# Performance work log

Measured on AMD Instinct MI355X. Metric: run time of the kernel, lower is better.

The kernel has to match this reference:

```python
import jax, jax.numpy as jnp
import numpy as np

B, NO, NR, DIM, RNN = 64, 128, 512, 1024, 1000


def setup_inputs() -> dict:
    key = jax.random.key(0)
    ks = jax.random.split(key, 32)
    def rn(k, shape, s=0.02):
        return jax.random.normal(k, shape, dtype=jnp.float32) * s
    inp = {}
    inp['obj_labels'] = jax.random.randint(ks[0], (B, NO, 1), 0, 26)
    inp['obj_masks'] = jnp.ones((B, NO), jnp.float32)
    inp['rela_masks'] = jnp.ones((B, NR), jnp.float32)
    inp['rela_edges'] = jax.random.randint(ks[1], (B, NR, 2), 0, NO)
    inp['rela_feats'] = jax.random.normal(ks[2], (B, NR, 8), dtype=jnp.float32)
    inp['box_feats'] = jax.random.normal(ks[3], (B, NO, 5), dtype=jnp.float32)
    # parameters
    inp['emb_table'] = jax.random.uniform(ks[4], (26, 128), jnp.float32, -0.1, 0.1)
    inp['w_objfeat'] = rn(ks[5], (5, 128));        inp['b_objfeat'] = jnp.zeros((128,), jnp.float32)
    inp['w_cat'] = rn(ks[6], (256, 128));          inp['b_cat'] = jnp.zeros((128,), jnp.float32)
    inp['w_obj'] = rn(ks[7], (128, RNN));          inp['b_obj'] = jnp.zeros((RNN,), jnp.float32)
    inp['w_rela'] = rn(ks[8], (8, RNN));           inp['b_rela'] = jnp.zeros((RNN,), jnp.float32)
    inp['w_gnn'] = rn(ks[9], (3 * RNN, RNN));      inp['b_gnn'] = jnp.zeros((RNN,), jnp.float32)
    inp['w_att_obj'] = rn(ks[10], (RNN, 1));       inp['b_att_obj'] = jnp.zeros((1,), jnp.float32)
    inp['w_att_rela'] = rn(ks[11], (RNN, 1));      inp['b_att_rela'] = jnp.zeros((1,), jnp.float32)
    inp['w_read'] = rn(ks[12], (2 * RNN, DIM));    inp['b_read'] = jnp.zeros((DIM,), jnp.float32)
    inp['w_fc'] = rn(ks[13], (DIM, 32 * 14 * 6));  inp['b_fc'] = jnp.zeros((32 * 14 * 6,), jnp.float32)
    inp['wt1'] = rn(ks[14], (32, 25, 3, 3));       inp['bt1'] = jnp.zeros((25,), jnp.float32)
    inp['wt2'] = rn(ks[15], (25, 25, 3, 3));       inp['bt2'] = jnp.zeros((25,), jnp.float32)
    inp['wt3'] = rn(ks[16], (25, 25, 3, 3));       inp['bt3'] = jnp.zeros((25,), jnp.float32)
    inp['wt4'] = rn(ks[17], (25, 25, 3, 3));       inp['bt4'] = jnp.zeros((25,), jnp.float32)
    return inp


def _attn(feats, mask, w, b):
    # feats: (B, N, RNN); mask: (B, N)
    dot = (jnp.tanh(feats) @ w + b)[..., 0]              # (B, N)
    wgt = jax.nn.softmax(dot, axis=1) * mask
    wgt = wgt / jnp.sum(wgt, axis=1, keepdims=True)
    return jnp.einsum('bn,bnd->bd', wgt, feats)          # (B, RNN)


def _up2(x):
    return jnp.repeat(jnp.repeat(x, 2, axis=2), 2, axis=3)


def _convT(x, w, b):
    # torch ConvTranspose2d (stride=1, pad=0) == full-padded corr with flipped kernel
    k = jnp.transpose(w, (1, 0, 2, 3))[:, :, ::-1, ::-1]  # (out, in, 3, 3)
    y = jax.lax.conv_general_dilated(x, k, (1, 1), [(2, 2), (2, 2)],
                                     dimension_numbers=('NCHW', 'OIHW', 'NCHW'))
    return y + b[None, :, None, None]


def reference(obj_labels, obj_masks, rela_masks, rela_edges, rela_feats, box_feats,
              emb_table, w_objfeat, b_objfeat, w_cat, b_cat, w_obj, b_obj,
              w_rela, b_rela, w_gnn, b_gnn, w_att_obj, b_att_obj,
              w_att_rela, b_att_rela, w_read, b_read, w_fc, b_fc,
              wt1, bt1, wt2, bt2, wt3, bt3, wt4, bt4):
    relu = jax.nn.relu
    # embeddings (dropout = identity at inference)
    obj_embed = relu(emb_table[obj_labels])[:, :, 0, :]                   # (B, NO, 128)
    obj_f = relu(box_feats @ w_objfeat + b_objfeat)                       # (B, NO, 128)
    obj_embed = relu(jnp.concatenate([obj_f, obj_embed], -1) @ w_cat + b_cat)
    obj_vecs = relu(obj_embed @ w_obj + b_obj)                            # (B, NO, 1000)
    rela_vecs = relu(rela_feats @ w_rela + b_rela)                        # (B, NR, 1000)
    # GNN: gather endpoints, concat, linear+relu, mask
    s = jnp.take_along_axis(obj_vecs, rela_edges[:, :, 0:1], axis=1)      # (B, NR, 1000)
    o = jnp.take_along_axis(obj_vecs, rela_edges[:, :, 1:2], axis=1)
    t = jnp.concatenate([s, rela_vecs, o], axis=-1)                       # (B, NR, 3000)
    new_rela = relu(t @ w_gnn + b_gnn) * rela_masks[..., None]
    # attention pooling
    a_obj = _attn(obj_vecs, obj_masks, w_att_obj, b_att_obj)
    a_rel = _attn(new_rela, rela_masks, w_att_rela, b_att_rela)
    enc = relu(jnp.concatenate([a_obj, a_rel], axis=1) @ w_read + b_read)  # (B, DIM)
    # decoder
    x = (enc @ w_fc + b_fc).reshape(-1, 32, 14, 6)
    x = relu(_convT(_up2(x), wt1, bt1))
    x = relu(_convT(_up2(x), wt2, bt2))
    x = relu(_convT(_up2(x), wt3, bt3))
    x = relu(_convT(_up2(x), wt4, bt4))
    x = jax.nn.sigmoid(x)                                                  # (B, 25, 254, 126)
    return enc, x
```

## Files before the change

### kernel.cpp

```cpp
#include <hip/hip_runtime.h>
#include <hip/hip_bf16.h>
#include <hip/hip_fp16.h>

#define B_    64
#define NO_   128
#define NR_   512
#define RNN_  1000
#define DIM_  1024

typedef short short8 __attribute__((ext_vector_type(8)));
typedef float f32x4  __attribute__((ext_vector_type(4)));
typedef float f32x2v __attribute__((ext_vector_type(2)));
typedef float f32x4v __attribute__((ext_vector_type(4)));

static __device__ __forceinline__ float bf2f(unsigned short u) {
    union { unsigned int i; float f; } x; x.i = ((unsigned int)u) << 16; return x.f;
}
static __device__ __forceinline__ short f2bf_s(float f) {
    __hip_bfloat16 h = __float2bfloat16(f);
    return *reinterpret_cast<short*>(&h);
}

#define GLOAD_LDS16(gp, lp) \
    __builtin_amdgcn_global_load_lds((const __attribute__((address_space(1))) void*)(gp), \
                                     (__attribute__((address_space(3))) void*)(lp), 16, 0, 0)

__global__ void k_obj_embed(const int* __restrict__ labels,
                            const float* __restrict__ box_feats,
                            const float* __restrict__ emb_table,
                            const float* __restrict__ w_objfeat, const float* __restrict__ b_objfeat,
                            const float* __restrict__ w_cat, const float* __restrict__ b_cat,
                            __hip_bfloat16* __restrict__ out)
{
    const int row = blockIdx.x;
    const int tid = threadIdx.x;
    __shared__ __align__(16) float cat[256];
    __shared__ float bf[5];
    if (tid < 5) bf[tid] = box_feats[row * 5 + tid];
    __syncthreads();
    float acc = b_objfeat[tid];
#pragma unroll
    for (int k = 0; k < 5; ++k) acc += bf[k] * w_objfeat[k * 128 + tid];
    cat[tid] = fmaxf(acc, 0.f);
    const int label = labels[row];
    cat[128 + tid] = fmaxf(emb_table[label * 128 + tid], 0.f);
    __syncthreads();
    float acc2 = b_cat[tid];
#pragma unroll 4
    for (int k4 = 0; k4 < 64; ++k4) {
        const f32x4 c4 = *(const f32x4*)&cat[k4 * 4];
        acc2 += c4[0] * w_cat[(k4 * 4 + 0) * 128 + tid];
        acc2 += c4[1] * w_cat[(k4 * 4 + 1) * 128 + tid];
        acc2 += c4[2] * w_cat[(k4 * 4 + 2) * 128 + tid];
        acc2 += c4[3] * w_cat[(k4 * 4 + 3) * 128 + tid];
    }
    out[(size_t)row * 128 + tid] = __float2bfloat16(fmaxf(acc2, 0.f));
}

__global__ void k_transpose(const float* __restrict__ W, __hip_bfloat16* __restrict__ Wt,
                            int K, int N, int ldn, int Kpad)
{
    __shared__ float t[32][33];
    const int k0 = blockIdx.x * 32, n0 = blockIdx.y * 32;
    const int c = threadIdx.x & 31, r8 = threadIdx.x >> 5;
#pragma unroll
    for (int rr = r8; rr < 32; rr += 8) {
        int k = k0 + rr, n = n0 + c;
        t[rr][c] = (k < K && n < N) ? W[(size_t)k * ldn + n] : 0.f;
    }
    __syncthreads();
#pragma unroll
    for (int rr = r8; rr < 32; rr += 8)
        Wt[(size_t)(n0 + rr) * Kpad + k0 + c] = __float2bfloat16(t[c][rr]);
}

__global__ void k_weff(const float* __restrict__ w, float* __restrict__ wg, int IC, int OC)
{
    const int idx = blockIdx.x * 256 + threadIdx.x;
    if (idx >= IC * OC) return;
    const float* wp = w + (size_t)idx * 9;
    float wl[9];
#pragma unroll
    for (int k = 0; k < 9; ++k) wl[k] = wp[k];
    const float rm_[2][2][3] = {{{0.f,1.f,1.f},{1.f,0.f,0.f}},
                                {{0.f,0.f,1.f},{1.f,1.f,0.f}}};
    float* o = wg + (size_t)idx * 16;
#pragma unroll
    for (int py = 0; py < 2; ++py)
#pragma unroll
    for (int px = 0; px < 2; ++px)
#pragma unroll
    for (int r = 0; r < 2; ++r)
#pragma unroll
    for (int c = 0; c < 2; ++c) {
        float s = 0.f;
#pragma unroll
        for (int ky = 0; ky < 3; ++ky)
#pragma unroll
        for (int kx = 0; kx < 3; ++kx)
            s += rm_[py][r][ky] * rm_[px][c][kx] * wl[ky * 3 + kx];
        o[(r * 2 + c) * 4 + (py * 2 + px)] = s;
    }
}

__global__ void k_zero_border(float* __restrict__ buf, int PH, int PW, int IR0, int IR1, int IC0, int IC1)
{
    float* plane = buf + (size_t)blockIdx.x * PH * PW;
    const int tid = threadIdx.x;
    const int topN = IR0 * PW;
    for (int i = tid; i < topN; i += 256) plane[i] = 0.f;
    const int botBase = IR1 * PW, botN = (PH - IR1) * PW;
    for (int i = tid; i < botN; i += 256) plane[botBase + i] = 0.f;
    const int rows = IR1 - IR0;
    const int wL = IC0, wR = PW - IC1, wLR = wL + wR;
    const int n = rows * wLR;
    for (int i = tid; i < n; i += 256) {
        const int r = i / wLR, c = i - r * wLR;
        const int col = (c < wL) ? c : (IC1 + c - wL);
        plane[(IR0 + r) * PW + col] = 0.f;
    }
}

__global__ void k_rv(const float* __restrict__ rela_feats, const float* __restrict__ w_rela,
                     const float* __restrict__ b_rela, __hip_bfloat16* __restrict__ rv)
{
    const int tid = threadIdx.x;
    const int r0 = blockIdx.x * 16;
    __shared__ float rf[16][8];
    if (tid < 128) rf[tid >> 3][tid & 7] = rela_feats[(size_t)(r0 + (tid >> 3)) * 8 + (tid & 7)];
    __syncthreads();
    const int row = r0 + (tid >> 4);
    const int cg = (tid & 15) * 64;
    float rloc[8];
#pragma unroll
    for (int f = 0; f < 8; ++f) rloc[f] = rf[tid >> 4][f];
    __hip_bfloat16* orow = rv + (size_t)row * 1024;
#pragma unroll
    for (int ch = 0; ch < 8; ++ch) {
        const int c = cg + ch * 8;
        float a[8];
        if (c < RNN_) {
            const float4 b0 = *(const float4*)(b_rela + c);
            const float4 b1 = *(const float4*)(b_rela + c + 4);
            a[0] = b0.x; a[1] = b0.y; a[2] = b0.z; a[3] = b0.w;
            a[4] = b1.x; a[5] = b1.y; a[6] = b1.z; a[7] = b1.w;
#pragma unroll
            for (int f = 0; f < 8; ++f) {
                const float4 w0 = *(const float4*)(w_rela + f * RNN_ + c);
                const float4 w1 = *(const float4*)(w_rela + f * RNN_ + c + 4);
                const float rfv = rloc[f];
                a[0] += rfv * w0.x; a[1] += rfv * w0.y; a[2] += rfv * w0.z; a[3] += rfv * w0.w;
                a[4] += rfv * w1.x; a[5] += rfv * w1.y; a[6] += rfv * w1.z; a[7] += rfv * w1.w;
            }
#pragma unroll
            for (int j = 0; j < 8; ++j) a[j] = fmaxf(a[j], 0.f);
        } else {
#pragma unroll
            for (int j = 0; j < 8; ++j) a[j] = 0.f;
        }
        short8 pk;
#pragma unroll
        for (int j = 0; j < 8; ++j) pk[j] = f2bf_s(a[j]);
        *(short8*)(orow + c) = pk;
    }
}

template<int MODE>
__global__ __launch_bounds__(256)
void mfma_gemm(const __hip_bfloat16* __restrict__ A, const __hip_bfloat16* __restrict__ Bt, int Kpad,
               const float* __restrict__ bias, int ldc, int ncols,
               __hip_bfloat16* __restrict__ outB,
               const __half* __restrict__ P13H, const int* __restrict__ edges,
               const float* __restrict__ masks, int lgNT)
{
    __shared__ __align__(16) ushort smem[16384];
    ushort* lA0 = smem;
    ushort* lA1 = smem + 4096;
    ushort* lB0 = smem + 8192;
    ushort* lB1 = smem + 12288;
    const int tid = threadIdx.x;
    const int l = (blockIdx.x & 7) * ((int)gridDim.x >> 3) + ((int)blockIdx.x >> 3);
    const int n0 = (l & ((1 << lgNT) - 1)) * 128;
    const int m0 = (l >> lgNT) * 128;
    const int wave = tid >> 6, lane = tid & 63;
    const int wr = wave >> 1, wc = wave & 1;
    const int lr = lane >> 4, lc = lane & 15;
    const int lrow = lane >> 2;
    const int lcol = (lane & 3) * 8;
    f32x4 acc[4][4];
#pragma unroll
    for (int i = 0; i < 4; ++i)
#pragma unroll
        for (int j = 0; j < 4; ++j) acc[i][j] = (f32x4){0.f, 0.f, 0.f, 0.f};

    for (int k0 = 0; k0 < Kpad; k0 += 64) {
        __syncthreads();
#pragma unroll
        for (int j = 0; j < 2; ++j) {
            const int rbase = j * 64 + wave * 16;
            GLOAD_LDS16(A  + (size_t)(m0 + rbase + lrow) * Kpad + k0 + lcol,      &lA0[rbase * 32]);
            GLOAD_LDS16(A  + (size_t)(m0 + rbase + lrow) * Kpad + k0 + 32 + lcol, &lA1[rbase * 32]);
            GLOAD_LDS16(Bt + (size_t)(n0 + rbase + lrow) * Kpad + k0 + lcol,      &lB0[rbase * 32]);
            GLOAD_LDS16(Bt + (size_t)(n0 + rbase + lrow) * Kpad + k0 + 32 + lcol, &lB1[rbase * 32]);
        }
        __syncthreads();
#pragma unroll
        for (int h = 0; h < 2; ++h) {
            const ushort* hA = h ? lA1 : lA0;
            const ushort* hB = h ? lB1 : lB0;
            short8 af[4], bfr[4];
#pragma unroll
            for (int mi = 0; mi < 4; ++mi)
                af[mi] = *(const short8*)&hA[(wr * 64 + mi * 16 + lc) * 32 + lr * 8];
#pragma unroll
            for (int ni = 0; ni < 4; ++ni)
                bfr[ni] = *(const short8*)&hB[(wc * 64 + ni * 16 + lc) * 32 + lr * 8];
#pragma unroll
            for (int mi = 0; mi < 4; ++mi)
#pragma unroll
                for (int ni = 0; ni < 4; ++ni)
                    acc[mi][ni] = __builtin_amdgcn_mfma_f32_16x16x32_bf16(af[mi], bfr[ni], acc[mi][ni], 0, 0, 0);
        }
    }

    float* ftile = (float*)smem;
    const int erow = tid >> 3;
    const int ecol0 = (tid & 7) * 16;
#pragma unroll
    for (int mi = 0; mi < 4; ++mi) {
        __syncthreads();
#pragma unroll
        for (int ni = 0; ni < 4; ++ni) {
            const int colL = wc * 64 + ni * 16 + lc;
#pragma unroll
            for (int r = 0; r < 4; ++r)
                ftile[(wr * 16 + lr * 4 + r) * 136 + colL] = acc[mi][ni][r];
        }
        __syncthreads();
        const int rowL = (erow < 16) ? (mi * 16 + erow) : (64 + mi * 16 + (erow - 16));
        const int grow = m0 + rowL;
        const int gcol = n0 + ecol0;
        float v[16];
#pragma unroll
        for (int j = 0; j < 4; ++j) {
            const f32x4 t4 = *(const f32x4*)&ftile[erow * 136 + ecol0 + j * 4];
            v[j*4+0] = t4[0]; v[j*4+1] = t4[1]; v[j*4+2] = t4[2]; v[j*4+3] = t4[3];
        }
        if (MODE == 0) {
            short8 pk0, pk1;
#pragma unroll
            for (int j = 0; j < 16; ++j) {
                const int c = gcol + j;
                const float bb = (c < ncols) ? bias[c] : 0.f;
                const short s = f2bf_s(fmaxf(v[j] + bb, 0.f));
                if (j < 8) pk0[j] = s; else pk1[j - 8] = s;
            }
            *(short8*)(outB + (size_t)grow * 1024 + gcol)     = pk0;
            *(short8*)(outB + (size_t)grow * 1024 + gcol + 8) = pk1;
        } else if (MODE == 1) {
            __half* outH = (__half*)outB;
            if (gcol + 15 < ncols) {
                __half h[16];
#pragma unroll
                for (int j = 0; j < 16; ++j) h[j] = __float2half(v[j]);
                *(short8*)(outH + (size_t)grow * ldc + gcol)     = *(short8*)&h[0];
                *(short8*)(outH + (size_t)grow * ldc + gcol + 8) = *(short8*)&h[8];
            } else {
#pragma unroll
                for (int j = 0; j < 16; ++j) {
                    const int c = gcol + j;
                    if (c < ncols) outH[(size_t)grow * ldc + c] = __float2half(v[j]);
                }
            }
        } else {
            const int b = grow >> 9;
            const int e0 = edges[grow * 2], e1 = edges[grow * 2 + 1];
            const float mk = masks[grow];
            const __half* p0 = P13H + (size_t)(b * NO_ + e0) * 2048 + gcol;
            const __half* p1 = P13H + (size_t)(b * NO_ + e1) * 2048 + 1024 + gcol;
            if (gcol + 15 < ncols) {
                __half h0[16], h1[16];
                *(short8*)&h0[0] = *(const short8*)p0;  *(short8*)&h0[8] = *(const short8*)(p0 + 8);
                *(short8*)&h1[0] = *(const short8*)p1;  *(short8*)&h1[8] = *(const short8*)(p1 + 8);
                float bb[16];
#pragma unroll
                for (int j = 0; j < 4; ++j) {
                    const float4 b4 = *(const float4*)(bias + gcol + j * 4);
                    bb[j*4+0] = b4.x; bb[j*4+1] = b4.y; bb[j*4+2] = b4.z; bb[j*4+3] = b4.w;
                }
                short8 pk0, pk1;
#pragma unroll
                for (int j = 0; j < 16; ++j) {
                    float val = v[j] + bb[j] + __half2float(h0[j]) + __half2float(h1[j]);
                    const short s = f2bf_s(fmaxf(val, 0.f) * mk);
                    if (j < 8) pk0[j] = s; else pk1[j - 8] = s;
                }
                *(short8*)(outB + (size_t)grow * RNN_ + gcol)     = pk0;
                *(short8*)(outB + (size_t)grow * RNN_ + gcol + 8) = pk1;
            } else if (gcol < ncols) {
#pragma unroll
                for (int j = 0; j < 16; ++j) {
                    const int c = gcol + j;
                    if (c < ncols) {
                        float val = v[j] + bias[c] + __half2float(p0[j]) + __half2float(p1[j]);
                        outB[(size_t)grow * RNN_ + c] = __float2bfloat16(fmaxf(val, 0.f) * mk);
                    }
                }
            }
        }
    }
}

__global__ void k_gemm_sk(const float* __restrict__ A, const float* __restrict__ W,
                          float* __restrict__ part, int N, int K, int ldw, int Kc)
{
    __shared__ float As[16][68];
    __shared__ float Ws[16][68];
    const int tid = threadIdx.x;
    const int n0 = blockIdx.x * 64;
    const int kz = blockIdx.y;
    const int kstart = kz * Kc;
    const int kend = (kstart + Kc < K) ? (kstart + Kc) : K;
    const int ty = tid >> 4, tx = tid & 15;
    float acc[4][4] = {};
    for (int k0 = kstart; k0 < kend; k0 += 16) {
#pragma unroll
        for (int i = 0; i < 4; ++i) {
            int lin = i * 256 + tid;
            int r = lin >> 4, kk = lin & 15;
            int k = k0 + kk;
            As[kk][r] = (k < kend) ? A[(size_t)r * K + k] : 0.f;
            int kr = lin >> 6, c = lin & 63;
            int kw = k0 + kr, cc = n0 + c;
            Ws[kr][c] = (kw < kend && cc < N) ? W[(size_t)kw * ldw + cc] : 0.f;
        }
        __syncthreads();
#pragma unroll
        for (int kk = 0; kk < 16; ++kk) {
            const float4 av = *reinterpret_cast<const float4*>(&As[kk][ty * 4]);
            const float4 wv = *reinterpret_cast<const float4*>(&Ws[kk][tx * 4]);
            const float a4[4] = {av.x, av.y, av.z, av.w};
            const float w4[4] = {wv.x, wv.y, wv.z, wv.w};
#pragma unroll
            for (int i = 0; i < 4; ++i)
#pragma unroll
                for (int j = 0; j < 4; ++j) acc[i][j] += a4[i] * w4[j];
        }
        __syncthreads();
    }
#pragma unroll
    for (int i = 0; i < 4; ++i) {
        const int row = ty * 4 + i;
#pragma unroll
        for (int j = 0; j < 4; ++j) {
            const int col = n0 + tx * 4 + j;
            if (col < N)
                part[((size_t)kz * 64 + row) * N + col] = acc[i][j];
        }
    }
}

__global__ void k_sk_reduce(const float* __restrict__ part, const float* __restrict__ bias,
                            float* __restrict__ out, int N, int KS, int ldo, int act)
{
    const int idx = blockIdx.x * 256 + threadIdx.x;
    if (idx >= 64 * N) return;
    const int row = idx / N, col = idx - row * N;
    float s = bias[col];
    for (int z = 0; z < KS; ++z) s += part[((size_t)z * 64 + row) * N + col];
    if (act) s = fmaxf(s, 0.f);
    out[(size_t)row * ldo + col] = s;
}

__global__ void k_att_dot(const __hip_bfloat16* __restrict__ feats, const float* __restrict__ w_att,
                          const float* __restrict__ b_att, float* __restrict__ dot, int D, int ld)
{
    const int row = blockIdx.x;
    const int tid = threadIdx.x;
    const int c = tid * 4;
    float s = 0.f;
    if (c < D) {
        const ushort4 v = *(const ushort4*)(feats + (size_t)row * ld + c);
        const float4 wv = *(const float4*)(w_att + c);
        s  = tanhf(bf2f(v.x)) * wv.x;
        s += tanhf(bf2f(v.y)) * wv.y;
        s += tanhf(bf2f(v.z)) * wv.z;
        s += tanhf(bf2f(v.w)) * wv.w;
    }
#pragma unroll
    for (int o = 32; o > 0; o >>= 1) s += __shfl_down(s, o, 64);
    __shared__ float part[4];
    if ((tid & 63) == 0) part[tid >> 6] = s;
    __syncthreads();
    if (tid == 0) dot[row] = part[0] + part[1] + part[2] + part[3] + b_att[0];
}

__global__ void k_softmax(const float* __restrict__ dot, const float* __restrict__ mask,
                          float* __restrict__ wgt, int Nn)
{
    const int b = blockIdx.x, tid = threadIdx.x;
    __shared__ float red[512];
    float v = dot[b * Nn + tid];
    red[tid] = v; __syncthreads();
    for (int s = Nn >> 1; s > 0; s >>= 1) { if (tid < s) red[tid] = fmaxf(red[tid], red[tid + s]); __syncthreads(); }
    float mx = red[0]; __syncthreads();
    float e = expf(v - mx);
    red[tid] = e; __syncthreads();
    for (int s = Nn >> 1; s > 0; s >>= 1) { if (tid < s) red[tid] += red[tid + s]; __syncthreads(); }
    float sm = red[0]; __syncthreads();
    float w0 = (e / sm) * mask[b * Nn + tid];
    red[tid] = w0; __syncthreads();
    for (int s = Nn >> 1; s > 0; s >>= 1) { if (tid < s) red[tid] += red[tid + s]; __syncthreads(); }
    wgt[b * Nn + tid] = w0 / red[0];
}

__global__ void k_wsum(const __hip_bfloat16* __restrict__ feats, const float* __restrict__ wgt,
                       float* __restrict__ out, int Nn, int D, int ld, int ldo, int off)
{
    const int b = blockIdx.x;
    const int tid = threadIdx.x;
    __shared__ float wl[512];
    for (int i = tid; i < Nn; i += 256) wl[i] = wgt[b * Nn + i];
    __syncthreads();
    const int d0 = tid * 4;
    if (d0 >= D) return;
    float a0 = 0.f, a1 = 0.f, a2 = 0.f, a3 = 0.f;
    const __hip_bfloat16* fp = feats + (size_t)b * Nn * ld + d0;
#pragma unroll 8
    for (int n = 0; n < Nn; ++n) {
        const ushort4 v = *(const ushort4*)(fp + (size_t)n * ld);
        const float w = wl[n];
        a0 += w * bf2f(v.x); a1 += w * bf2f(v.y);
        a2 += w * bf2f(v.z); a3 += w * bf2f(v.w);
    }
    *(float4*)(out + (size_t)b * ldo + off + d0) = make_float4(a0, a1, a2, a3);
}

__global__ void k_convt5(const float* __restrict__ src, const float* __restrict__ wg,
                         const float* __restrict__ bias, float* __restrict__ dst,
                         int IC, int OC, int SH, int SW, int act,
                         int dro, int dco, int DPH, int DPW)
{
    const int QH = SH + 1, QW = SW + 1;
    const int ocg = blockIdx.y, b = blockIdx.z;
    const int tid = threadIdx.x;
    const int p = blockIdx.x * blockDim.x + tid;
    if (p >= QH * QW) return;
    const int a = p / QW, g = p % QW;
    const bool rm = (a > 0), rp = (a < SH);
    const bool cm = (g > 0), cp = (g < SW);
    f32x2v acc2[5][2];
#pragma unroll
    for (int ol = 0; ol < 5; ++ol) { acc2[ol][0] = (f32x2v){0.f, 0.f}; acc2[ol][1] = (f32x2v){0.f, 0.f}; }
    const float* sb = src + (size_t)(b * IC) * SH * SW;
    const int base = (a - 1) * SW + (g - 1);
    for (int ic = 0; ic < IC; ++ic) {
        const float* s = sb + (size_t)ic * SH * SW;
        const float s00 = (rm && cm) ? s[base] : 0.f;
        const float s01 = (rm && cp) ? s[base + 1] : 0.f;
        const float s10 = (rp && cm) ? s[base + SW] : 0.f;
        const float s11 = (rp && cp) ? s[base + SW + 1] : 0.f;
        const f32x2v b0 = {s00, s00}, b1 = {s01, s01}, b2 = {s10, s10}, b3 = {s11, s11};
        const float* wf = wg + ((size_t)ic * OC + ocg * 5) * 16;
#pragma unroll
        for (int ol = 0; ol < 5; ++ol) {
            const f32x4v w0 = *(const f32x4v*)(wf + ol * 16 + 0);
            const f32x4v w1 = *(const f32x4v*)(wf + ol * 16 + 4);
            const f32x4v w2 = *(const f32x4v*)(wf + ol * 16 + 8);
            const f32x4v w3 = *(const f32x4v*)(wf + ol * 16 + 12);
            acc2[ol][0] += b0 * __builtin_shufflevector(w0, w0, 0, 1);
            acc2[ol][0] += b1 * __builtin_shufflevector(w1, w1, 0, 1);
            acc2[ol][0] += b2 * __builtin_shufflevector(w2, w2, 0, 1);
            acc2[ol][0] += b3 * __builtin_shufflevector(w3, w3, 0, 1);
            acc2[ol][1] += b0 * __builtin_shufflevector(w0, w0, 2, 3);
            acc2[ol][1] += b1 * __builtin_shufflevector(w1, w1, 2, 3);
            acc2[ol][1] += b2 * __builtin_shufflevector(w2, w2, 2, 3);
            acc2[ol][1] += b3 * __builtin_shufflevector(w3, w3, 2, 3);
        }
    }
#pragma unroll
    for (int ol = 0; ol < 5; ++ol) {
        const int oc = ocg * 5 + ol;
        const float bv = bias[oc];
        float a00 = acc2[ol][0].x + bv, a01 = acc2[ol][0].y + bv;
        float a10 = acc2[ol][1].x + bv, a11 = acc2[ol][1].y + bv;
        if (act == 1) {
            a00 = fmaxf(a00, 0.f); a01 = fmaxf(a01, 0.f);
            a10 = fmaxf(a10, 0.f); a11 = fmaxf(a11, 0.f);
        } else {
            a00 = 1.f / (1.f + expf(-a00)); a01 = 1.f / (1.f + expf(-a01));
            a10 = 1.f / (1.f + expf(-a10)); a11 = 1.f / (1.f + expf(-a11));
        }
        float* dp = dst + ((size_t)(b * OC + oc) * DPH + 2 * a + dro) * DPW + 2 * g + dco;
        *reinterpret_cast<float2*>(dp)       = make_float2(a00, a01);
        *reinterpret_cast<float2*>(dp + DPW) = make_float2(a10, a11);
    }
}

__global__ void k_convtv(const float* __restrict__ src, int SPP, int SPW,
                         const float* __restrict__ wg,
                         const float* __restrict__ bias, float* __restrict__ dst,
                         int IC, int OC, int QH, int QW, int act, int LG,
                         int dro, int dco, int DPH, int DPW)
{
    const int ocg = blockIdx.y, b = blockIdx.z;
    const int tid = threadIdx.x;
    const int g = tid & ((1 << LG) - 1);
    const int a0 = blockIdx.x * ((256 >> LG) * 2) + (tid >> LG) * 2;
    if (g >= QW || a0 >= QH) return;
    float acc[5][2][4];
#pragma unroll
    for (int ol = 0; ol < 5; ++ol)
#pragma unroll
        for (int q = 0; q < 2; ++q)
#pragma unroll
            for (int j = 0; j < 4; ++j) acc[ol][q][j] = 0.f;
    const float* sb = src + (size_t)(b * IC) * SPP;
    const int rbase = a0 * SPW + g + 1;
    for (int ic = 0; ic < IC; ++ic) {
        const float* s = sb + (size_t)ic * SPP;
        float sv[3][2];
#pragma unroll
        for (int i = 0; i < 3; ++i) {
            sv[i][0] = s[rbase + i * SPW];
            sv[i][1] = s[rbase + i * SPW + 1];
        }
        const float* wf = wg + ((size_t)ic * OC + ocg * 5) * 16;
#pragma unroll
        for (int ol = 0; ol < 5; ++ol) {
#pragma unroll
            for (int q = 0; q < 2; ++q) {
#pragma unroll
                for (int j = 0; j < 4; ++j) {
                    acc[ol][q][j] += sv[q][0]     * wf[ol * 16 +  0 + j];
                    acc[ol][q][j] += sv[q][1]     * wf[ol * 16 +  4 + j];
                    acc[ol][q][j] += sv[q + 1][0] * wf[ol * 16 +  8 + j];
                    acc[ol][q][j] += sv[q + 1][1] * wf[ol * 16 + 12 + j];
                }
            }
        }
    }
    const bool q1ok = (a0 + 1 < QH);
#pragma unroll
    for (int ol = 0; ol < 5; ++ol) {
        const int oc = ocg * 5 + ol;
        const float bv = bias[oc];
        float* dp0 = dst + ((size_t)(b * OC + oc) * DPH + 2 * a0 + dro) * DPW + 2 * g + dco;
#pragma unroll
        for (int q = 0; q < 2; ++q) {
            if (q == 1 && !q1ok) continue;
            float v0 = acc[ol][q][0] + bv, v1 = acc[ol][q][1] + bv;
            float v2 = acc[ol][q][2] + bv, v3 = acc[ol][q][3] + bv;
            if (act == 1) {
                v0 = fmaxf(v0, 0.f); v1 = fmaxf(v1, 0.f);
                v2 = fmaxf(v2, 0.f); v3 = fmaxf(v3, 0.f);
            } else {
                v0 = 1.f / (1.f + expf(-v0)); v1 = 1.f / (1.f + expf(-v1));
                v2 = 1.f / (1.f + expf(-v2)); v3 = 1.f / (1.f + expf(-v3));
            }
            float* dp = dp0 + q * 2 * DPW;
            *reinterpret_cast<float2*>(dp)       = make_float2(v0, v1);
            *reinterpret_cast<float2*>(dp + DPW) = make_float2(v2, v3);
        }
    }
}

extern "C" void kernel_launch(void* const* d_in, const int* in_sizes, int n_in,
                              void* d_out, int out_size, void* d_ws, size_t ws_size,
                              hipStream_t stream)
{
    const int*   obj_labels = (const int*)  d_in[0];
    const float* obj_masks  = (const float*)d_in[1];
    const float* rela_masks = (const float*)d_in[2];
    const int*   rela_edges = (const int*)  d_in[3];
    const float* rela_feats = (const float*)d_in[4];
    const float* box_feats  = (const float*)d_in[5];
    const float* emb_table  = (const float*)d_in[6];
    const float* w_objfeat  = (const float*)d_in[7];
    const float* b_objfeat  = (const float*)d_in[8];
    const float* w_cat      = (const float*)d_in[9];
    const float* b_cat      = (const float*)d_in[10];
    const float* w_obj      = (const float*)d_in[11];
    const float* b_obj      = (const float*)d_in[12];
    const float* w_rela     = (const float*)d_in[13];
    const float* b_rela     = (const float*)d_in[14];
    const float* w_gnn      = (const float*)d_in[15];
    const float* b_gnn      = (const float*)d_in[16];
    const float* w_att_obj  = (const float*)d_in[17];
    const float* b_att_obj  = (const float*)d_in[18];
    const float* w_att_rela = (const float*)d_in[19];
    const float* b_att_rela = (const float*)d_in[20];
    const float* w_read     = (const float*)d_in[21];
    const float* b_read     = (const float*)d_in[22];
    const float* w_fc       = (const float*)d_in[23];
    const float* b_fc       = (const float*)d_in[24];
    const float* wt1 = (const float*)d_in[25]; const float* bt1 = (const float*)d_in[26];
    const float* wt2 = (const float*)d_in[27]; const float* bt2 = (const float*)d_in[28];
    const float* wt3 = (const float*)d_in[29]; const float* bt3 = (const float*)d_in[30];
    const float* wt4 = (const float*)d_in[31]; const float* bt4 = (const float*)d_in[32];

    float* ws = (float*)d_ws;
    __hip_bfloat16* objembB  = (__hip_bfloat16*)(ws);
    __hip_bfloat16* obj_vecsB= (__hip_bfloat16*)(ws + 524288);
    __hip_bfloat16* w_objT   = (__hip_bfloat16*)(ws + 4718592);
    __hip_bfloat16* w1T      = (__hip_bfloat16*)(ws + 4784128);
    __hip_bfloat16* w3T      = (__hip_bfloat16*)(ws + 5308416);
    __hip_bfloat16* w2T      = (__hip_bfloat16*)(ws + 5832704);
    __half*         P13H     = (__half*)(ws + 6356992);
    __hip_bfloat16* rvB      = (__hip_bfloat16*)(ws + 14745600);
    __hip_bfloat16* newRB    = (__hip_bfloat16*)(ws + 31522816);
    float* dot_obj = ws + 47906816;
    float* dot_rel = dot_obj + 8192;
    float* wgt_obj = dot_rel + 32768;
    float* wgt_rel = wgt_obj + 8192;
    float* a_cat   = wgt_rel + 32768;
    float* part_enc = a_cat + 128000;
    float* part_fc  = part_enc + 524288;
    float* weff1 = ws + 50017184;
    float* weff2 = weff1 + 12800;
    float* weff3 = weff2 + 10000;
    float* weff4 = weff3 + 10000;
    float* d0  = ws;
    float* d1  = ws + 6356992;
    float* d2p = ws + 7028992;
    float* d3p = ws + 10619392;
    float* enc  = (float*)d_out;
    float* xout = (float*)d_out + 65536;

    k_transpose<<<dim3(4, 32),  256, 0, stream>>>(w_obj, w_objT, 128, RNN_, RNN_, 128);
    k_transpose<<<dim3(32, 32), 256, 0, stream>>>(w_gnn,                      w1T, RNN_, RNN_, RNN_, 1024);
    k_transpose<<<dim3(32, 32), 256, 0, stream>>>(w_gnn + (size_t)2*RNN_*RNN_,w3T, RNN_, RNN_, RNN_, 1024);
    k_transpose<<<dim3(32, 32), 256, 0, stream>>>(w_gnn + (size_t)RNN_*RNN_,  w2T, RNN_, RNN_, RNN_, 1024);
    k_weff<<<dim3(4), 256, 0, stream>>>(wt1, weff1, 32, 25);
    k_weff<<<dim3(3), 256, 0, stream>>>(wt2, weff2, 25, 25);
    k_weff<<<dim3(3), 256, 0, stream>>>(wt3, weff3, 25, 25);
    k_weff<<<dim3(3), 256, 0, stream>>>(wt4, weff4, 25, 25);
    k_obj_embed<<<dim3(8192), dim3(128), 0, stream>>>(obj_labels, box_feats, emb_table,
                                                      w_objfeat, b_objfeat, w_cat, b_cat, objembB);
    mfma_gemm<0><<<dim3(512), 256, 0, stream>>>(objembB, w_objT, 128, b_obj,
                                                0, RNN_, obj_vecsB, nullptr, nullptr, nullptr, 3);
    mfma_gemm<1><<<dim3(1024), 256, 0, stream>>>(obj_vecsB, w1T, 1024, nullptr,
                                                 2048, 2048, (__hip_bfloat16*)P13H, nullptr, nullptr, nullptr, 4);
    k_rv<<<dim3(2048), 256, 0, stream>>>(rela_feats, w_rela, b_rela, rvB);
    mfma_gemm<2><<<dim3(2048), 256, 0, stream>>>(rvB, w2T, 1024, b_gnn,
                                                 0, RNN_, newRB, P13H, rela_edges, rela_masks, 3);
    k_att_dot<<<8192,  256, 0, stream>>>(obj_vecsB, w_att_obj,  b_att_obj,  dot_obj, RNN_, 1024);
    k_att_dot<<<32768, 256, 0, stream>>>(newRB,     w_att_rela, b_att_rela, dot_rel, RNN_, RNN_);
    k_softmax<<<64, 128, 0, stream>>>(dot_obj, obj_masks,  wgt_obj, 128);
    k_softmax<<<64, 512, 0, stream>>>(dot_rel, rela_masks, wgt_rel, 512);
    k_wsum<<<dim3(64), 256, 0, stream>>>(obj_vecsB, wgt_obj, a_cat, 128, RNN_, 1024, 2000, 0);
    k_wsum<<<dim3(64), 256, 0, stream>>>(newRB,     wgt_rel, a_cat, 512, RNN_, RNN_, 2000, RNN_);
    k_gemm_sk<<<dim3(16, 8), 256, 0, stream>>>(a_cat, w_read, part_enc, DIM_, 2000, DIM_, 256);
    k_sk_reduce<<<dim3(256), 256, 0, stream>>>(part_enc, b_read, enc, DIM_, 8, DIM_, 1);
    k_gemm_sk<<<dim3(42, 8), 256, 0, stream>>>(enc, w_fc, part_fc, 2688, DIM_, 2688, 128);
    k_sk_reduce<<<dim3(672), 256, 0, stream>>>(part_fc, b_fc, d0, 2688, 8, 2688, 0);
    k_zero_border<<<dim3(1600), 256, 0, stream>>>(d2p, 66, 34, 1, 63, 2, 32);
    k_zero_border<<<dim3(1600), 256, 0, stream>>>(d3p, 130, 66, 1, 127, 2, 64);
    k_convt5<<<dim3(1, 5, 64), 256, 0, stream>>>(d0, weff1, bt1, d1, 32, 25, 14, 6, 1, 0, 0, 30, 14);
    k_convt5<<<dim3(2, 5, 64), 256, 0, stream>>>(d1, weff2, bt2, d2p, 25, 25, 30, 14, 1, 1, 2, 66, 34);
    k_convtv<<<dim3(4, 5, 64), 256, 0, stream>>>(d2p, 66 * 34, 34, weff3, bt3, d3p,
                                                 25, 25, 63, 31, 1, 5, 1, 2, 130, 66);
    k_convtv<<<dim3(16, 5, 64), 256, 0, stream>>>(d3p, 130 * 66, 66, weff4, bt4, xout,
                                                  25, 25, 127, 63, 2, 6, 0, 0, 254, 126);
}
```

Before: 757.8 us.

## Run final transposed conv as bf16 MFMA GEMM over NHWC-packed input

Replaces the last scalar transposed-conv kernel with an implicit GEMM on MFMA bf16 instructions. The padded activation is first repacked to NHWC bf16 with channels padded to 32, and the effective weights are packed into a bf16 B matrix. The GEMM fuses bias, ReLU-free sigmoid and the 2x2 sub-pixel scatter in its epilogue. This targets the largest decoder layer's FP32 ALU cost, at the price of an extra repack pass and bf16 rounding of inputs and weights.

```diff
diff --git a/kernel.cpp b/kernel.cpp
--- a/kernel.cpp
+++ b/kernel.cpp
@@ -103,6 +103,26 @@
     }
 }
 
+__global__ void k_weffB(const float* __restrict__ weff, __hip_bfloat16* __restrict__ Bt4)
+{
+    const int t = blockIdx.x * 256 + threadIdx.x;
+    if (t >= 512) return;
+    const int s = t >> 7, n = t & 127;
+    const int oc = n >> 2, j = n & 3;
+    ushort* dst = (ushort*)Bt4 + (size_t)t * 32;
+#pragma unroll
+    for (int icb = 0; icb < 4; ++icb) {
+        short8 pk;
+#pragma unroll
+        for (int u = 0; u < 8; ++u) {
+            const int ic = icb * 8 + u;
+            const float v = (ic < 25 && oc < 25) ? weff[((size_t)ic * 25 + oc) * 16 + s * 4 + j] : 0.f;
+            pk[u] = f2bf_s(v);
+        }
+        *(short8*)(dst + icb * 8) = pk;
+    }
+}
+
 __global__ void k_zero_border(float* __restrict__ buf, int PH, int PW, int IR0, int IR1, int IC0, int IC1)
 {
     float* plane = buf + (size_t)blockIdx.x * PH * PW;
@@ -118,6 +138,27 @@
         const int r = i / wLR, c = i - r * wLR;
         const int col = (c < wL) ? c : (IC1 + c - wL);
         plane[(IR0 + r) * PW + col] = 0.f;
+    }
+}
+
+__global__ void k_nhwc(const float* __restrict__ src, __hip_bfloat16* __restrict__ dst)
+{
+    const int idx = blockIdx.x * 256 + threadIdx.x;
+    const int b = idx / 8580;
+    const int rem = idx - b * 8580;
+    const int p = rem / 66, q = rem - (rem / 66) * 66;
+    const float* sp = src + ((size_t)b * 25 * 130 + p) * 66 + q;
+    ushort* dp = (ushort*)dst + (size_t)idx * 32;
+#pragma unroll
+    for (int icb = 0; icb < 4; ++icb) {
+        short8 pk;
+#pragma unroll
+        for (int u = 0; u < 8; ++u) {
+            const int ic = icb * 8 + u;
+            const float v = (ic < 25) ? sp[(size_t)ic * 130 * 66] : 0.f;
+            pk[u] = f2bf_s(v);
+        }
+        *(short8*)(dp + icb * 8) = pk;
     }
 }
 
@@ -305,6 +346,97 @@
                         float val = v[j] + bias[c] + __half2float(p0[j]) + __half2float(p1[j]);
                         outB[(size_t)grow * RNN_ + c] = __float2bfloat16(fmaxf(val, 0.f) * mk);
                     }
+                }
+            }
+        }
+    }
+}
+
+__global__ __launch_bounds__(256)
+void mfma_conv4(const __hip_bfloat16* __restrict__ nhwc, const __hip_bfloat16* __restrict__ Bt4,
+                const float* __restrict__ bias, float* __restrict__ xout)
+{
+    __shared__ __align__(16) ushort smem[16384];
+    const int tid = threadIdx.x;
+    const int m0 = (int)blockIdx.x * 128;
+    const int wave = tid >> 6, lane = tid & 63;
+    const int wr = wave >> 1, wc = wave & 1;
+    const int lr = lane >> 4, lc = lane & 15;
+    const int lrow = lane >> 2;
+    const int lcol = (lane & 3) * 8;
+    f32x4 acc[4][4];
+#pragma unroll
+    for (int i = 0; i < 4; ++i)
+#pragma unroll
+        for (int j = 0; j < 4; ++j) acc[i][j] = (f32x4){0.f, 0.f, 0.f, 0.f};
+
+#pragma unroll
+    for (int s = 0; s < 4; ++s) {
+        const int sr = s >> 1, sc = s & 1;
+#pragma unroll
+        for (int j = 0; j < 2; ++j) {
+            const int rbase = j * 64 + wave * 16;
+            const int row = m0 + rbase + lrow;
+            const int b = row >> 13, a = (row >> 6) & 127, g = row & 63;
+            GLOAD_LDS16(nhwc + ((size_t)(b * 130 + a + sr) * 66 + (g + 1 + sc)) * 32 + lcol,
+                        &smem[s * 4096 + rbase * 32]);
+        }
+    }
+    __syncthreads();
+#pragma unroll
+    for (int s = 0; s < 4; ++s) {
+        const ushort* lA = &smem[s * 4096];
+        short8 af[4], bfr[4];
+#pragma unroll
+        for (int mi = 0; mi < 4; ++mi)
+            af[mi] = *(const short8*)&lA[(wr * 64 + mi * 16 + lc) * 32 + lr * 8];
+#pragma unroll
+        for (int ni = 0; ni < 4; ++ni)
+            bfr[ni] = *(const short8*)((const ushort*)Bt4 +
+                      ((size_t)(s * 128 + wc * 64 + ni * 16 + lc)) * 32 + lr * 8);
+#pragma unroll
+        for (int mi = 0; mi < 4; ++mi)
+#pragma unroll
+            for (int ni = 0; ni < 4; ++ni)
+                acc[mi][ni] = __builtin_amdgcn_mfma_f32_16x16x32_bf16(af[mi], bfr[ni], acc[mi][ni], 0, 0, 0);
+    }
+
+    float* ftile = (float*)smem;
+    const int erow = tid >> 3;
+    const int ecol0 = (tid & 7) * 16;
+#pragma unroll
+    for (int mi = 0; mi < 4; ++mi) {
+        __syncthreads();
+#pragma unroll
+        for (int ni = 0; ni < 4; ++ni) {
+            const int colL = wc * 64 + ni * 16 + lc;
+#pragma unroll
+            for (int r = 0; r < 4; ++r)
+                ftile[(wr * 16 + lr * 4 + r) * 136 + colL] = acc[mi][ni][r];
+        }
+        __syncthreads();
+        const int rowL = (erow < 16) ? (mi * 16 + erow) : (64 + mi * 16 + (erow - 16));
+        const int grow = m0 + rowL;
+        const int b = grow >> 13, a = (grow >> 6) & 127, g = grow & 63;
+        float v[16];
+#pragma unroll
+        for (int j = 0; j < 4; ++j) {
+            const f32x4 t4 = *(const f32x4*)&ftile[erow * 136 + ecol0 + j * 4];
+            v[j*4+0] = t4[0]; v[j*4+1] = t4[1]; v[j*4+2] = t4[2]; v[j*4+3] = t4[3];
+        }
+        if (a < 127 && g < 63) {
+#pragma unroll
+            for (int k = 0; k < 4; ++k) {
+                const int oc = (ecol0 >> 2) + k;
+                if (oc < 25) {
+                    const float bv = bias[oc];
+                    const float j0 = 1.f / (1.f + expf(-(v[k*4+0] + bv)));
+                    const float j1 = 1.f / (1.f + expf(-(v[k*4+1] + bv)));
+                    const float j2 = 1.f / (1.f + expf(-(v[k*4+2] + bv)));
+                    const float j3 = 1.f / (1.f + expf(-(v[k*4+3] + bv)));
+                    float* dp = xout + ((size_t)(b * 25 + oc) * 254 + 2 * a) * 126 + 2 * g;
+                    *reinterpret_cast<float2*>(dp)       = make_float2(j0, j1);
+                    *reinterpret_cast<float2*>(dp + 126) = make_float2(j2, j3);
                 }
             }
         }
@@ -620,10 +752,12 @@
     float* weff2 = weff1 + 12800;
     float* weff3 = weff2 + 10000;
     float* weff4 = weff3 + 10000;
+    __hip_bfloat16* Bt4 = (__hip_bfloat16*)(ws + 50059984);
     float* d0  = ws;
     float* d1  = ws + 6356992;
     float* d2p = ws + 7028992;
     float* d3p = ws + 10619392;
+    __hip_bfloat16* nhwc4 = (__hip_bfloat16*)(ws + 24347392);
     float* enc  = (float*)d_out;
     float* xout = (float*)d_out + 65536;
 
@@ -635,6 +769,7 @@
     k_weff<<<dim3(3), 256, 0, stream>>>(wt2, weff2, 25, 25);
     k_weff<<<dim3(3), 256, 0, stream>>>(wt3, weff3, 25, 25);
     k_weff<<<dim3(3), 256, 0, stream>>>(wt4, weff4, 25, 25);
+    k_weffB<<<dim3(2), 256, 0, stream>>>(weff4, Bt4);
     k_obj_embed<<<dim3(8192), dim3(128), 0, stream>>>(obj_labels, box_feats, emb_table,
                                                       w_objfeat, b_objfeat, w_cat, b_cat, objembB);
     mfma_gemm<0><<<dim3(512), 256, 0, stream>>>(objembB, w_objT, 128, b_obj,
@@ -660,6 +795,6 @@
     k_convt5<<<dim3(2, 5, 64), 256, 0, stream>>>(d1, weff2, bt2, d2p, 25, 25, 30, 14, 1, 1, 2, 66, 34);
     k_convtv<<<dim3(4, 5, 64), 256, 0, stream>>>(d2p, 66 * 34, 34, weff3, bt3, d3p,
                                                  25, 25, 63, 31, 1, 5, 1, 2, 130, 66);
-    k_convtv<<<dim3(16, 5, 64), 256, 0, stream>>>(d3p, 130 * 66, 66, weff4, bt4, xout,
-                                                  25, 25, 127, 63, 2, 6, 0, 0, 254, 126);
-}
+    k_nhwc<<<dim3(2145), 256, 0, stream>>>(d3p, nhwc4);
+    mfma_conv4<<<dim3(4096), 256, 0, stream>>>(nhwc4, Bt4, bt4, xout);
+}
```

After: 764.8 us. About the same (+0.9%).
